# Optimization experiments

Measured on AMD Instinct MI355X. Metric: run time of the kernel, lower is better.

## Reference

```python
import jax, jax.numpy as jnp
import numpy as np

COORD_DIM = 2
ENTITY_DIM = 1024
FIELD_DIM = 512
INPUT_DIM = 512
NUM_ENTITIES = 512
FIELD_RESOLUTION = 10000  # grid_size = 100


def _gelu(x):
    return jax.nn.gelu(x, approximate=False)  # torch nn.GELU default (erf)


def setup_inputs() -> dict:
    key = jax.random.key(0)
    ks = jax.random.split(key, 9)
    std = 0.02  # matches _init_parameters
    B, S = 8, 4096
    x = jax.random.normal(ks[0], (B, S, INPUT_DIM), dtype=jnp.float32)
    # DensityField: density_projection = Linear(D,F) GELU Linear(F,F) GELU; coordinate_generator = Linear(F,2)
    W1 = jax.random.normal(ks[1], (INPUT_DIM, FIELD_DIM), jnp.float32) * std
    b1 = jnp.zeros((FIELD_DIM,), jnp.float32)
    W2 = jax.random.normal(ks[2], (FIELD_DIM, FIELD_DIM), jnp.float32) * std
    b2 = jnp.zeros((FIELD_DIM,), jnp.float32)
    Wc = jax.random.normal(ks[3], (FIELD_DIM, COORD_DIM), jnp.float32) * std
    bc = jnp.zeros((COORD_DIM,), jnp.float32)
    # entity_mapper: Linear(F+2, F) GELU Linear(F, E+2+1)
    We1 = jax.random.normal(ks[4], (FIELD_DIM + COORD_DIM, FIELD_DIM), jnp.float32) * std
    be1 = jnp.zeros((FIELD_DIM,), jnp.float32)
    We2 = jax.random.normal(ks[5], (FIELD_DIM, ENTITY_DIM + COORD_DIM + 1), jnp.float32) * std
    be2 = jnp.zeros((ENTITY_DIM + COORD_DIM + 1,), jnp.float32)
    # output_projection: Linear(E, 2E) GELU Linear(2E, D)
    Wo1 = jax.random.normal(ks[6], (ENTITY_DIM, 2 * ENTITY_DIM), jnp.float32) * std
    bo1 = jnp.zeros((2 * ENTITY_DIM,), jnp.float32)
    Wo2 = jax.random.normal(ks[7], (2 * ENTITY_DIM, INPUT_DIM), jnp.float32) * std
    bo2 = jnp.zeros((INPUT_DIM,), jnp.float32)
    return dict(x=x, W1=W1, b1=b1, W2=W2, b2=b2, Wc=Wc, bc=bc,
                We1=We1, be1=be1, We2=We2, be2=be2,
                Wo1=Wo1, bo1=bo1, Wo2=Wo2, bo2=bo2)


def _forward(x, W1, b1, W2, b2, Wc, bc, We1, be1, We2, be2, Wo1, bo1, Wo2, bo2):
    # --- DensityField ---
    df = _gelu(_gelu(x @ W1 + b1) @ W2 + b2)          # [B,S,F]
    coords = df @ Wc + bc                              # [B,S,2]
    # --- ContinuousEntityExtractor ---
    field_input = jnp.concatenate([coords, df], axis=-1)          # [B,S,2+F]
    ef = _gelu(field_input @ We1 + be1) @ We2 + be2                # [B,S,E+3]
    importance = jnp.linalg.norm(ef, axis=-1)                      # [B,S]
    _, top_idx = jax.lax.top_k(importance, NUM_ENTITIES)           # [B,Ne]
    sel = jnp.take_along_axis(ef, top_idx[..., None], axis=1)     # [B,Ne,E+3]
    positions = sel[..., :COORD_DIM]                               # [B,Ne,2]
    states = sel[..., COORD_DIM:COORD_DIM + ENTITY_DIM]            # [B,Ne,E]
    # --- ContinuousOutputGenerator ---
    proj = _gelu(states @ Wo1 + bo1) @ Wo2 + bo2                   # [B,Ne,D]
    grid_size = int(FIELD_RESOLUTION ** 0.5)
    g = jnp.linspace(-1.0, 1.0, grid_size)
    gx, gy = jnp.meshgrid(g, g, indexing='ij')
    grid = jnp.stack([gx.ravel(), gy.ravel()], axis=-1)            # [G2,2]
    # squared euclidean distances via expansion (torch: cdist then **2)
    g2 = jnp.sum(grid * grid, axis=-1)                             # [G2]
    p2 = jnp.sum(positions * positions, axis=-1)                   # [B,Ne]
    gp = jnp.einsum('gc,bnc->bgn', grid, positions)                # [B,G2,Ne]
    sq = g2[None, :, None] + p2[:, None, :] - 2.0 * gp             # [B,G2,Ne]
    attn = jnp.exp(-sq / 0.1)
    attn = attn / (attn.sum(axis=-1, keepdims=True) + 1e-8)
    out = jnp.einsum('bgn,bnd->bgd', attn, proj)                   # [B,G2,D]
    return out


def reference(x, W1, b1, W2, b2, Wc, bc, We1, be1, We2, be2, Wo1, bo1, Wo2, bo2):
    return _forward(x, W1, b1, W2, b2, Wc, bc, We1, be1, We2, be2, Wo1, bo1, Wo2, bo2)
```

## Files before the change

### kernel.cpp

```cpp
#include <hip/hip_runtime.h>
#include <hip/hip_bf16.h>
#include <math.h>


typedef __attribute__((ext_vector_type(8))) short bf16x8;
typedef __attribute__((ext_vector_type(4))) float f32x4;

__device__ __forceinline__ float gelu_exact(float x) {
    return 0.5f * x * (1.0f + erff(x * 0.7071067811865476f));
}

__device__ __forceinline__ void async_copy16(const void* g, void* l) {
    __builtin_amdgcn_global_load_lds(
        (const __attribute__((address_space(1))) unsigned int*)g,
        (__attribute__((address_space(3))) unsigned int*)l, 16, 0, 0);
}

__global__ __launch_bounds__(256) void split_kernel(
    const float* __restrict__ in,
    __hip_bfloat16* __restrict__ hi, __hip_bfloat16* __restrict__ lo)
{
    const int i4 = blockIdx.x * 256 + threadIdx.x;
    const float4 v = ((const float4*)in)[i4];
    __hip_bfloat16 h0 = __float2bfloat16(v.x);
    __hip_bfloat16 h1 = __float2bfloat16(v.y);
    __hip_bfloat16 h2 = __float2bfloat16(v.z);
    __hip_bfloat16 h3 = __float2bfloat16(v.w);
    __hip_bfloat16 l0 = __float2bfloat16(v.x - __bfloat162float(h0));
    __hip_bfloat16 l1 = __float2bfloat16(v.y - __bfloat162float(h1));
    __hip_bfloat16 l2 = __float2bfloat16(v.z - __bfloat162float(h2));
    __hip_bfloat16 l3 = __float2bfloat16(v.w - __bfloat162float(h3));
    union { __hip_bfloat16 h[4]; short4 s; } uh, ul;
    uh.h[0] = h0; uh.h[1] = h1; uh.h[2] = h2; uh.h[3] = h3;
    ul.h[0] = l0; ul.h[1] = l1; ul.h[2] = l2; ul.h[3] = l3;
    ((short4*)hi)[i4] = uh.s;
    ((short4*)lo)[i4] = ul.s;
}

__global__ __launch_bounds__(256) void transpose_split_kernel(
    const float* __restrict__ in,
    __hip_bfloat16* __restrict__ outH, __hip_bfloat16* __restrict__ outL,
    int K, int N)
{
    __shared__ float tile[32][33];
    const int k0 = blockIdx.y * 32, n0 = blockIdx.x * 32;
    const int t = threadIdx.x;
    const int lr = t >> 5, lc = t & 31;
    #pragma unroll
    for (int p = 0; p < 4; p++) {
        const int r = p * 8 + lr;
        const int n = n0 + lc;
        tile[r][lc] = (n < N) ? in[(size_t)(k0 + r) * N + n] : 0.f;
    }
    __syncthreads();
    #pragma unroll
    for (int p = 0; p < 4; p++) {
        const int r = p * 8 + lr;
        const float v = tile[lc][r];
        const __hip_bfloat16 h = __float2bfloat16(v);
        const __hip_bfloat16 l = __float2bfloat16(v - __bfloat162float(h));
        outH[(size_t)(n0 + r) * K + k0 + lc] = h;
        outL[(size_t)(n0 + r) * K + k0 + lc] = l;
    }
}

__global__ __launch_bounds__(256) void init_kernel(
    float* __restrict__ IMP, float* __restrict__ CRD,
    const float* __restrict__ bc)
{
    const int t = blockIdx.x * 256 + threadIdx.x;
    IMP[t] = 0.f;
    ((float2*)CRD)[t] = make_float2(bc[0], bc[1]);
}

template<bool GELU, bool RANK2, bool SPLIT, bool BOUNDS, int FUSE>
__global__ __launch_bounds__(256, 4) void gemm3k(
    const __hip_bfloat16* __restrict__ Ahi, const __hip_bfloat16* __restrict__ Alo,
    const __hip_bfloat16* __restrict__ Bhi, const __hip_bfloat16* __restrict__ Blo,
    const float* __restrict__ bias,
    float* __restrict__ Cf, int ldc,
    __hip_bfloat16* __restrict__ Chi, __hip_bfloat16* __restrict__ Clo,
    int N,
    const float* __restrict__ A2, const float* __restrict__ W2r,
    float* __restrict__ FO, const float* __restrict__ Wc)
{
    constexpr int K = 512;
    constexpr int NPS = K / 32;
    constexpr int NSTEPS = 3 * NPS;
    __shared__ __align__(16) __hip_bfloat16 As[2][128][32];
    __shared__ __align__(16) __hip_bfloat16 Bs[2][128][32];
    const int t = threadIdx.x;
    const int wave = t >> 6, lane = t & 63;
    const int wave_m = wave >> 1, wave_n = wave & 1;
    const int fr = lane & 15, quad = lane >> 4;
    const int gx = gridDim.x;
    const int nwg = gx * gridDim.y;
    int lid = blockIdx.y * gx + blockIdx.x;
    if ((nwg & 7) == 0) {
        const int chunk = nwg >> 3;
        lid = (lid & 7) * chunk + (lid >> 3);
    }
    const int m0 = (lid / gx) * 128;
    const int n0 = (lid % gx) * 128;
    const int srow = lane >> 2;
    const int skc  = (lane & 3) * 8;

    f32x4 acc[4][4] = {};

    auto STAGE = [&](int buf, int step) {
        int seg = 0, ts = step;
        if (ts >= NPS) { ts -= NPS; seg = 1; }
        if (ts >= NPS) { ts -= NPS; seg = 2; }
        const int kk = ts << 5;
        const __hip_bfloat16* Ab = (seg == 2) ? Alo : Ahi;
        const __hip_bfloat16* Bb = (seg == 1) ? Blo : Bhi;
        #pragma unroll
        for (int s = 0; s < 2; s++) {
            const int r = wave * 32 + s * 16 + srow;
            async_copy16(Ab + (size_t)(m0 + r) * K + kk + skc,
                         &As[buf][wave * 32 + s * 16][0]);
            async_copy16(Bb + (size_t)(n0 + r) * K + kk + skc,
                         &Bs[buf][wave * 32 + s * 16][0]);
        }
    };

    STAGE(0, 0);
    __syncthreads();
    int cur = 0;
    for (int step = 0; step < NSTEPS; ++step) {
        if (step + 1 < NSTEPS) STAGE(cur ^ 1, step + 1);
        bf16x8 af[4], bfv[4];
        #pragma unroll
        for (int i = 0; i < 4; i++)
            af[i] = *(const bf16x8*)&As[cur][wave_m * 64 + i * 16 + fr][quad * 8];
        #pragma unroll
        for (int j = 0; j < 4; j++)
            bfv[j] = *(const bf16x8*)&Bs[cur][wave_n * 64 + j * 16 + fr][quad * 8];
        #pragma unroll
        for (int i = 0; i < 4; i++)
            #pragma unroll
            for (int j = 0; j < 4; j++)
                acc[i][j] = __builtin_amdgcn_mfma_f32_16x16x32_bf16(
                    af[i], bfv[j], acc[i][j], 0, 0, 0);
        __syncthreads();
        cur ^= 1;
    }

    #pragma unroll
    for (int i = 0; i < 4; i++) {
        const int gmb = m0 + wave_m * 64 + i * 16 + quad * 4;
        float a2x[4], a2y[4];
        if (RANK2) {
            #pragma unroll
            for (int r = 0; r < 4; r++) {
                a2x[r] = A2[(size_t)(gmb + r) * 2];
                a2y[r] = A2[(size_t)(gmb + r) * 2 + 1];
            }
        }
        float f0[4] = {0.f, 0.f, 0.f, 0.f};
        float f1[4] = {0.f, 0.f, 0.f, 0.f};
        #pragma unroll
        for (int j = 0; j < 4; j++) {
            const int gn = n0 + wave_n * 64 + j * 16 + fr;
            const bool nok = !BOUNDS || (gn < N);
            const float bv = nok ? bias[gn] : 0.f;
            float w2a = 0.f, w2b = 0.f;
            if (RANK2) { w2a = W2r[gn]; w2b = W2r[512 + gn]; }
            float wcx = 0.f, wcy = 0.f;
            if (FUSE == 1) {
                const float2 wc = ((const float2*)Wc)[gn];
                wcx = wc.x; wcy = wc.y;
            }
            #pragma unroll
            for (int r = 0; r < 4; r++) {
                const int gm = gmb + r;
                float v = acc[i][j][r] + bv;
                if (RANK2) v += a2x[r] * w2a + a2y[r] * w2b;
                if (GELU) v = gelu_exact(v);
                if (SPLIT) {
                    const __hip_bfloat16 h = __float2bfloat16(v);
                    const __hip_bfloat16 l =
                        __float2bfloat16(v - __bfloat162float(h));
                    Chi[(size_t)gm * 512 + gn] = h;
                    Clo[(size_t)gm * 512 + gn] = l;
                } else if (nok) {
                    Cf[(size_t)gm * ldc + gn] = v;
                }
                if (FUSE == 1) { f0[r] += v * wcx; f1[r] += v * wcy; }
                if (FUSE == 2 && nok) f0[r] += v * v;
            }
        }
        if (FUSE) {
            #pragma unroll
            for (int r = 0; r < 4; r++) {
                float a = f0[r], b = f1[r];
                #pragma unroll
                for (int off = 1; off < 16; off <<= 1) {
                    a += __shfl_xor(a, off);
                    if (FUSE == 1) b += __shfl_xor(b, off);
                }
                if (fr == 0) {
                    if (FUSE == 1) {
                        atomicAdd(&FO[(size_t)(gmb + r) * 2],     a);
                        atomicAdd(&FO[(size_t)(gmb + r) * 2 + 1], b);
                    } else {
                        atomicAdd(&FO[gmb + r], a);
                    }
                }
            }
        }
    }
}

__global__ __launch_bounds__(1024) void topk_kernel(
    const float* __restrict__ IMP, int* __restrict__ IDX)
{
    __shared__ float v[4096];
    __shared__ int   ix[4096];
    const int b = blockIdx.x, t = threadIdx.x;
    for (int i = t; i < 4096; i += 1024) {
        v[i] = sqrtf(IMP[b * 4096 + i]);
        ix[i] = i;
    }
    __syncthreads();
    for (int k = 2; k <= 4096; k <<= 1) {
        for (int j = k >> 1; j > 0; j >>= 1) {
            for (int q = 0; q < 4; q++) {
                const int i = t + (q << 10);
                const int l = i ^ j;
                if (l > i) {
                    const float vi = v[i], vl = v[l];
                    const int   ii = ix[i], il = ix[l];
                    const bool after = (vi < vl) || (vi == vl && ii > il);
                    const bool dirAsc = ((i & k) == 0);
                    if (dirAsc ? after : !after) {
                        v[i] = vl; v[l] = vi; ix[i] = il; ix[l] = ii;
                    }
                }
            }
            __syncthreads();
        }
    }
    if (t < 512) IDX[b * 512 + t] = ix[t];
}

__global__ __launch_bounds__(256) void gather_kernel(
    const float* __restrict__ EF, const int* __restrict__ IDX,
    float* __restrict__ POS, __hip_bfloat16* __restrict__ ST)
{
    const int bn  = blockIdx.x;
    const int b   = bn >> 9;
    const int row = IDX[bn];
    const float* src = EF + ((size_t)(b * 4096) + row) * 1027;
    const int t = threadIdx.x;
    if (t < 2) POS[(size_t)bn * 2 + t] = src[t];
    __hip_bfloat16* dst = ST + (size_t)bn * 1024;
    for (int k = t; k < 1024; k += 256) dst[k] = __float2bfloat16(src[2 + k]);
}

__global__ __launch_bounds__(256) void transpose_cvt_kernel(
    const float* __restrict__ in, __hip_bfloat16* __restrict__ out,
    int K, int N)
{
    __shared__ float tile[32][33];
    const int k0 = blockIdx.y * 32, n0 = blockIdx.x * 32;
    const int t = threadIdx.x;
    const int lr = t >> 5, lc = t & 31;
    #pragma unroll
    for (int p = 0; p < 4; p++) {
        const int r = p * 8 + lr;
        tile[r][lc] = in[(size_t)(k0 + r) * N + n0 + lc];
    }
    __syncthreads();
    #pragma unroll
    for (int p = 0; p < 4; p++) {
        const int r = p * 8 + lr;
        out[(size_t)(n0 + r) * K + k0 + lc] = __float2bfloat16(tile[lc][r]);
    }
}

__global__ __launch_bounds__(256) void transpose_proj_kernel(
    const __hip_bfloat16* __restrict__ in, __hip_bfloat16* __restrict__ out)
{
    __shared__ __hip_bfloat16 tile[32][33];
    const int b = blockIdx.z;
    const int n0 = blockIdx.y * 32, d0 = blockIdx.x * 32;
    const int t = threadIdx.x;
    const int lr = t >> 5, lc = t & 31;
    #pragma unroll
    for (int p = 0; p < 4; p++) {
        const int r = p * 8 + lr;
        tile[r][lc] = in[((size_t)b * 512 + n0 + r) * 512 + d0 + lc];
    }
    __syncthreads();
    #pragma unroll
    for (int p = 0; p < 4; p++) {
        const int r = p * 8 + lr;
        out[((size_t)b * 512 + d0 + r) * 512 + n0 + lc] = tile[lc][r];
    }
}

template<bool GELU>
__global__ __launch_bounds__(256, 4) void gemm_post(
    const __hip_bfloat16* __restrict__ A,
    const __hip_bfloat16* __restrict__ BT,
    const float* __restrict__ bias,
    __hip_bfloat16* __restrict__ C,
    int N, int K)
{
    __shared__ __align__(16) __hip_bfloat16 As[2][128][32];
    __shared__ __align__(16) __hip_bfloat16 Bs[2][128][32];
    const int t = threadIdx.x;
    const int wave = t >> 6, lane = t & 63;
    const int wave_m = wave >> 1, wave_n = wave & 1;
    const int fr = lane & 15, quad = lane >> 4;
    const int gx = gridDim.x;
    const int nwg = gx * gridDim.y;
    int lid = blockIdx.y * gx + blockIdx.x;
    if ((nwg & 7) == 0) {
        const int chunk = nwg >> 3;
        lid = (lid & 7) * chunk + (lid >> 3);
    }
    const int m0 = (lid / gx) * 128;
    const int n0 = (lid % gx) * 128;
    const int srow = lane >> 2;
    const int skc  = (lane & 3) * 8;
    const int nsteps = K >> 5;

    f32x4 acc[4][4] = {};

    auto STAGE = [&](int buf, int step) {
        const int kk = step << 5;
        #pragma unroll
        for (int s = 0; s < 2; s++) {
            const int r = wave * 32 + s * 16 + srow;
            async_copy16(A  + (size_t)(m0 + r) * K + kk + skc,
                         &As[buf][wave * 32 + s * 16][0]);
            async_copy16(BT + (size_t)(n0 + r) * K + kk + skc,
                         &Bs[buf][wave * 32 + s * 16][0]);
        }
    };

    STAGE(0, 0);
    __syncthreads();
    int cur = 0;
    for (int step = 0; step < nsteps; ++step) {
        if (step + 1 < nsteps) STAGE(cur ^ 1, step + 1);
        bf16x8 af[4], bfv[4];
        #pragma unroll
        for (int i = 0; i < 4; i++)
            af[i] = *(const bf16x8*)&As[cur][wave_m * 64 + i * 16 + fr][quad * 8];
        #pragma unroll
        for (int j = 0; j < 4; j++)
            bfv[j] = *(const bf16x8*)&Bs[cur][wave_n * 64 + j * 16 + fr][quad * 8];
        #pragma unroll
        for (int i = 0; i < 4; i++)
            #pragma unroll
            for (int j = 0; j < 4; j++)
                acc[i][j] = __builtin_amdgcn_mfma_f32_16x16x32_bf16(
                    af[i], bfv[j], acc[i][j], 0, 0, 0);
        __syncthreads();
        cur ^= 1;
    }
    #pragma unroll
    for (int i = 0; i < 4; i++) {
        const int gm = m0 + wave_m * 64 + i * 16 + quad * 4;
        #pragma unroll
        for (int j = 0; j < 4; j++) {
            const int gn = n0 + wave_n * 64 + j * 16 + fr;
            const float bv = bias[gn];
            #pragma unroll
            for (int r = 0; r < 4; r++) {
                float v = acc[i][j][r] + bv;
                if (GELU) v = gelu_exact(v);
                C[(size_t)(gm + r) * N + gn] = __float2bfloat16(v);
            }
        }
    }
}

__global__ __launch_bounds__(256) void attn_mfma_kernel(
    const float* __restrict__ POS,
    const __hip_bfloat16* __restrict__ PROJT,
    float* __restrict__ OUT)
{
    __shared__ __align__(16) __hip_bfloat16 Bs[256][32];
    __shared__ float2 pos_s[512];
    __shared__ float srow_s[4][16];
    const int t = threadIdx.x;
    const int wave = t >> 6, lane = t & 63;
    const int fr = lane & 15, quad = lane >> 4;
    const int b  = blockIdx.z;
    const int g0 = blockIdx.x * 64;
    const int d0 = blockIdx.y * 256;

    {
        const float2* p = (const float2*)(POS + (size_t)b * 512 * 2);
        pos_s[t]       = p[t];
        pos_s[256 + t] = p[256 + t];
    }
    const int g = g0 + wave * 16 + fr;
    const bool gv = g < 10000;
    const float step = 2.0f / 99.0f;
    const int gi = gv ? (g / 100) : 0;
    const int gj = gv ? (g - gi * 100) : 0;
    const float gx = -1.f + step * (float)gi;
    const float gy = -1.f + step * (float)gj;

    f32x4 acc[16] = {};
    float wsum = 0.f;
    __syncthreads();

    for (int n0 = 0; n0 < 512; n0 += 32) {
        #pragma unroll
        for (int s = 0; s < 4; s++) {
            const int seg = wave * 4 + s;
            const __hip_bfloat16* gB = PROJT
                + ((size_t)b * 512 + d0 + seg * 16 + (lane >> 2)) * 512
                + n0 + (lane & 3) * 8;
            async_copy16(gB, &Bs[seg * 16][0]);
        }
        bf16x8 wf;
        float wl = 0.f;
        #pragma unroll
        for (int j = 0; j < 8; j++) {
            const int n = n0 + quad * 8 + j;
            const float2 pn = pos_s[n];
            const float dx = gx - pn.x, dy = gy - pn.y;
            const float w = gv ? __expf(-10.0f * (dx * dx + dy * dy)) : 0.f;
            const __hip_bfloat16 wb = __float2bfloat16(w);
            union { __hip_bfloat16 h; short s; } u; u.h = wb;
            wf[j] = u.s;
            wl += __bfloat162float(wb);
        }
        wsum += wl;
        __syncthreads();
        #pragma unroll
        for (int j = 0; j < 16; j++) {
            const bf16x8 bv = *(const bf16x8*)&Bs[j * 16 + fr][quad * 8];
            acc[j] = __builtin_amdgcn_mfma_f32_16x16x32_bf16(wf, bv, acc[j], 0, 0, 0);
        }
        __syncthreads();
    }
    wsum += __shfl_xor(wsum, 16);
    wsum += __shfl_xor(wsum, 32);
    if (lane < 16) srow_s[wave][lane] = wsum;
    __syncthreads();
    const int rbase = quad * 4;
    float inv[4];
    #pragma unroll
    for (int r = 0; r < 4; r++)
        inv[r] = 1.0f / (srow_s[wave][rbase + r] + 1e-8f);
    #pragma unroll
    for (int j = 0; j < 16; j++) {
        const int col = d0 + j * 16 + fr;
        #pragma unroll
        for (int r = 0; r < 4; r++) {
            const int gr = g0 + wave * 16 + rbase + r;
            if (gr < 10000)
                OUT[((size_t)b * 10000 + gr) * 512 + col] = acc[j][r] * inv[r];
        }
    }
}

extern "C" void kernel_launch(void* const* d_in, const int* in_sizes, int n_in,
                              void* d_out, int out_size, void* d_ws, size_t ws_size,
                              hipStream_t stream)
{
    const float* x   = (const float*)d_in[0];
    const float* W1  = (const float*)d_in[1];
    const float* b1  = (const float*)d_in[2];
    const float* W2  = (const float*)d_in[3];
    const float* b2  = (const float*)d_in[4];
    const float* Wc  = (const float*)d_in[5];
    const float* bc  = (const float*)d_in[6];
    const float* We1 = (const float*)d_in[7];
    const float* be1 = (const float*)d_in[8];
    const float* We2 = (const float*)d_in[9];
    const float* be2 = (const float*)d_in[10];
    const float* Wo1 = (const float*)d_in[11];
    const float* bo1 = (const float*)d_in[12];
    const float* Wo2 = (const float*)d_in[13];
    const float* bo2 = (const float*)d_in[14];
    float* out = (float*)d_out;

    const size_t BS = 32768;
    const size_t ACT = BS * 512;
    __hip_bfloat16* P0h = (__hip_bfloat16*)d_ws;
    __hip_bfloat16* P0l = P0h + ACT;
    __hip_bfloat16* P1h = P0l + ACT;
    __hip_bfloat16* P1l = P1h + ACT;
    float* EF  = (float*)(P1l + ACT);
    float* CRD = EF + BS * 1027;
    float* IMP = CRD + BS * 2;
    int*   IDX = (int*)(IMP + BS);
    float* POS = (float*)(IDX + 4096);
    __hip_bfloat16* W1Th = (__hip_bfloat16*)(POS + 4096 * 2);
    __hip_bfloat16* W1Tl = W1Th + 512 * 512;
    __hip_bfloat16* W2Th = W1Tl + 512 * 512;
    __hip_bfloat16* W2Tl = W2Th + 512 * 512;
    __hip_bfloat16* We1Th = W2Tl + 512 * 512;
    __hip_bfloat16* We1Tl = We1Th + 512 * 512;
    __hip_bfloat16* We2Th = We1Tl + 512 * 512;
    __hip_bfloat16* We2Tl = We2Th + (size_t)1152 * 512;
    __hip_bfloat16* ST    = P0h;
    __hip_bfloat16* H4    = ST + (size_t)4096 * 1024;
    __hip_bfloat16* PROJ  = H4 + (size_t)4096 * 2048;
    __hip_bfloat16* PROJT = PROJ + (size_t)4096 * 512;
    __hip_bfloat16* Wo1T  = PROJT + (size_t)4096 * 512;
    __hip_bfloat16* Wo2T  = Wo1T + (size_t)2048 * 1024;

    dim3 blk(256);
    split_kernel<<<dim3(16384), blk, 0, stream>>>(x, P0h, P0l);
    transpose_split_kernel<<<dim3(16, 16), blk, 0, stream>>>(W1, W1Th, W1Tl, 512, 512);
    transpose_split_kernel<<<dim3(16, 16), blk, 0, stream>>>(W2, W2Th, W2Tl, 512, 512);
    transpose_split_kernel<<<dim3(16, 16), blk, 0, stream>>>(We1 + 2 * 512, We1Th, We1Tl, 512, 512);
    transpose_split_kernel<<<dim3(36, 16), blk, 0, stream>>>(We2, We2Th, We2Tl, 512, 1027);
    init_kernel<<<dim3(128), blk, 0, stream>>>(IMP, CRD, bc);
    gemm3k<true, false, true, false, 0><<<dim3(4, 256), blk, 0, stream>>>(
        P0h, P0l, W1Th, W1Tl, b1, nullptr, 0, P1h, P1l, 512,
        nullptr, nullptr, nullptr, nullptr);
    gemm3k<true, false, true, false, 1><<<dim3(4, 256), blk, 0, stream>>>(
        P1h, P1l, W2Th, W2Tl, b2, nullptr, 0, P0h, P0l, 512,
        nullptr, nullptr, CRD, Wc);
    gemm3k<true, true, true, false, 0><<<dim3(4, 256), blk, 0, stream>>>(
        P0h, P0l, We1Th, We1Tl, be1, nullptr, 0, P1h, P1l, 512,
        CRD, We1, nullptr, nullptr);
    gemm3k<false, false, false, true, 2><<<dim3(9, 256), blk, 0, stream>>>(
        P1h, P1l, We2Th, We2Tl, be2, EF, 1027, nullptr, nullptr, 1027,
        nullptr, nullptr, IMP, nullptr);
    topk_kernel<<<dim3(8), dim3(1024), 0, stream>>>(IMP, IDX);
    transpose_cvt_kernel<<<dim3(64, 32), blk, 0, stream>>>(Wo1, Wo1T, 1024, 2048);
    transpose_cvt_kernel<<<dim3(16, 64), blk, 0, stream>>>(Wo2, Wo2T, 2048, 512);
    gather_kernel<<<dim3(4096), blk, 0, stream>>>(EF, IDX, POS, ST);
    gemm_post<true><<<dim3(16, 32), blk, 0, stream>>>(
        ST, Wo1T, bo1, H4, 2048, 1024);
    gemm_post<false><<<dim3(4, 32), blk, 0, stream>>>(
        H4, Wo2T, bo2, PROJ, 512, 2048);
    transpose_proj_kernel<<<dim3(16, 16, 8), blk, 0, stream>>>(PROJ, PROJT);
    attn_mfma_kernel<<<dim3(157, 2, 8), blk, 0, stream>>>(POS, PROJT, out);
}
```

Baseline: 898.4 us.

## Restructure split-bf16 GEMMs, store entity features as bf16, double-buffer attention

The 3-pass split-bf16 GEMM now loads hi and lo tiles of A and B together and issues all three MFMA products per K step, instead of running 48 sequential segments. This removes redundant hi tile reloads and the per-step segment logic, at the cost of double the LDS footprint and a launch-bounds occupancy hint lowered from 4 to 2. The last entity GEMM writes the 1024 state columns as bf16 and the coordinates separately, which shrinks the EF buffer and lets the gather kernel do a plain copy. All GEMMs switch to a fragment-contiguous LDS layout and wrap the MFMA block in s_setprio. The attention kernel gains double-buffered PROJT staging, which removes one barrier per iteration.

```diff
diff --git a/kernel.cpp b/kernel.cpp
--- a/kernel.cpp
+++ b/kernel.cpp
@@ -73,22 +73,21 @@
     ((float2*)CRD)[t] = make_float2(bc[0], bc[1]);
 }
 
-template<bool GELU, bool RANK2, bool SPLIT, bool BOUNDS, int FUSE>
-__global__ __launch_bounds__(256, 4) void gemm3k(
+template<bool GELU, bool RANK2, bool EFMODE, bool FUSEC>
+__global__ __launch_bounds__(256, 2) void gemm3k(
     const __hip_bfloat16* __restrict__ Ahi, const __hip_bfloat16* __restrict__ Alo,
     const __hip_bfloat16* __restrict__ Bhi, const __hip_bfloat16* __restrict__ Blo,
     const float* __restrict__ bias,
-    float* __restrict__ Cf, int ldc,
     __hip_bfloat16* __restrict__ Chi, __hip_bfloat16* __restrict__ Clo,
-    int N,
+    __hip_bfloat16* __restrict__ EFB, float* __restrict__ EFC,
+    float* __restrict__ IMP,
     const float* __restrict__ A2, const float* __restrict__ W2r,
-    float* __restrict__ FO, const float* __restrict__ Wc)
-{
-    constexpr int K = 512;
-    constexpr int NPS = K / 32;
-    constexpr int NSTEPS = 3 * NPS;
-    __shared__ __align__(16) __hip_bfloat16 As[2][128][32];
-    __shared__ __align__(16) __hip_bfloat16 Bs[2][128][32];
+    float* __restrict__ CRD, const float* __restrict__ Wc)
+{
+    __shared__ __align__(16) __hip_bfloat16 AsH[2][4096];
+    __shared__ __align__(16) __hip_bfloat16 AsL[2][4096];
+    __shared__ __align__(16) __hip_bfloat16 BsH[2][4096];
+    __shared__ __align__(16) __hip_bfloat16 BsL[2][4096];
     const int t = threadIdx.x;
     const int wave = t >> 6, lane = t & 63;
     const int wave_m = wave >> 1, wave_n = wave & 1;
@@ -96,52 +95,69 @@
     const int gx = gridDim.x;
     const int nwg = gx * gridDim.y;
     int lid = blockIdx.y * gx + blockIdx.x;
-    if ((nwg & 7) == 0) {
+    {
         const int chunk = nwg >> 3;
         lid = (lid & 7) * chunk + (lid >> 3);
     }
     const int m0 = (lid / gx) * 128;
     const int n0 = (lid % gx) * 128;
-    const int srow = lane >> 2;
-    const int skc  = (lane & 3) * 8;
+    const int lrow   = lane & 15;
+    const int lchunk = (lane >> 4) * 8;
 
     f32x4 acc[4][4] = {};
 
     auto STAGE = [&](int buf, int step) {
-        int seg = 0, ts = step;
-        if (ts >= NPS) { ts -= NPS; seg = 1; }
-        if (ts >= NPS) { ts -= NPS; seg = 2; }
-        const int kk = ts << 5;
-        const __hip_bfloat16* Ab = (seg == 2) ? Alo : Ahi;
-        const __hip_bfloat16* Bb = (seg == 1) ? Blo : Bhi;
+        const int kk = step << 5;
         #pragma unroll
         for (int s = 0; s < 2; s++) {
-            const int r = wave * 32 + s * 16 + srow;
-            async_copy16(Ab + (size_t)(m0 + r) * K + kk + skc,
-                         &As[buf][wave * 32 + s * 16][0]);
-            async_copy16(Bb + (size_t)(n0 + r) * K + kk + skc,
-                         &Bs[buf][wave * 32 + s * 16][0]);
+            const int seg = wave * 2 + s;
+            const size_t ao = (size_t)(m0 + seg * 16 + lrow) * 512 + kk + lchunk;
+            const size_t bo = (size_t)(n0 + seg * 16 + lrow) * 512 + kk + lchunk;
+            async_copy16(Ahi + ao, &AsH[buf][seg * 512]);
+            async_copy16(Alo + ao, &AsL[buf][seg * 512]);
+            async_copy16(Bhi + bo, &BsH[buf][seg * 512]);
+            async_copy16(Blo + bo, &BsL[buf][seg * 512]);
         }
     };
 
     STAGE(0, 0);
     __syncthreads();
     int cur = 0;
-    for (int step = 0; step < NSTEPS; ++step) {
-        if (step + 1 < NSTEPS) STAGE(cur ^ 1, step + 1);
-        bf16x8 af[4], bfv[4];
-        #pragma unroll
-        for (int i = 0; i < 4; i++)
-            af[i] = *(const bf16x8*)&As[cur][wave_m * 64 + i * 16 + fr][quad * 8];
-        #pragma unroll
-        for (int j = 0; j < 4; j++)
-            bfv[j] = *(const bf16x8*)&Bs[cur][wave_n * 64 + j * 16 + fr][quad * 8];
+    const int abase = wave_m * 2048 + quad * 128 + fr * 8;
+    const int bbase = wave_n * 2048 + quad * 128 + fr * 8;
+    for (int step = 0; step < 16; ++step) {
+        if (step + 1 < 16) STAGE(cur ^ 1, step + 1);
+        bf16x8 ah[4], al[4], bh[4], bl[4];
+        #pragma unroll
+        for (int i = 0; i < 4; i++) {
+            ah[i] = *(const bf16x8*)&AsH[cur][abase + i * 512];
+            al[i] = *(const bf16x8*)&AsL[cur][abase + i * 512];
+        }
+        #pragma unroll
+        for (int j = 0; j < 4; j++) {
+            bh[j] = *(const bf16x8*)&BsH[cur][bbase + j * 512];
+            bl[j] = *(const bf16x8*)&BsL[cur][bbase + j * 512];
+        }
+        __builtin_amdgcn_s_setprio(1);
         #pragma unroll
         for (int i = 0; i < 4; i++)
             #pragma unroll
             for (int j = 0; j < 4; j++)
                 acc[i][j] = __builtin_amdgcn_mfma_f32_16x16x32_bf16(
-                    af[i], bfv[j], acc[i][j], 0, 0, 0);
+                    ah[i], bh[j], acc[i][j], 0, 0, 0);
+        #pragma unroll
+        for (int i = 0; i < 4; i++)
+            #pragma unroll
+            for (int j = 0; j < 4; j++)
+                acc[i][j] = __builtin_amdgcn_mfma_f32_16x16x32_bf16(
+                    ah[i], bl[j], acc[i][j], 0, 0, 0);
+        #pragma unroll
+        for (int i = 0; i < 4; i++)
+            #pragma unroll
+            for (int j = 0; j < 4; j++)
+                acc[i][j] = __builtin_amdgcn_mfma_f32_16x16x32_bf16(
+                    al[i], bh[j], acc[i][j], 0, 0, 0);
+        __builtin_amdgcn_s_setprio(0);
         __syncthreads();
         cur ^= 1;
     }
@@ -162,12 +178,12 @@
         #pragma unroll
         for (int j = 0; j < 4; j++) {
             const int gn = n0 + wave_n * 64 + j * 16 + fr;
-            const bool nok = !BOUNDS || (gn < N);
+            const bool nok = !EFMODE || (gn < 1027);
             const float bv = nok ? bias[gn] : 0.f;
             float w2a = 0.f, w2b = 0.f;
             if (RANK2) { w2a = W2r[gn]; w2b = W2r[512 + gn]; }
             float wcx = 0.f, wcy = 0.f;
-            if (FUSE == 1) {
+            if (FUSEC) {
                 const float2 wc = ((const float2*)Wc)[gn];
                 wcx = wc.x; wcy = wc.y;
             }
@@ -177,34 +193,36 @@
                 float v = acc[i][j][r] + bv;
                 if (RANK2) v += a2x[r] * w2a + a2y[r] * w2b;
                 if (GELU) v = gelu_exact(v);
-                if (SPLIT) {
+                if (EFMODE) {
+                    if (gn < 2) EFC[(size_t)gm * 2 + gn] = v;
+                    else if (gn < 1026)
+                        EFB[(size_t)gm * 1024 + gn - 2] = __float2bfloat16(v);
+                    if (nok) f0[r] += v * v;
+                } else {
                     const __hip_bfloat16 h = __float2bfloat16(v);
                     const __hip_bfloat16 l =
                         __float2bfloat16(v - __bfloat162float(h));
                     Chi[(size_t)gm * 512 + gn] = h;
                     Clo[(size_t)gm * 512 + gn] = l;
-                } else if (nok) {
-                    Cf[(size_t)gm * ldc + gn] = v;
+                    if (FUSEC) { f0[r] += v * wcx; f1[r] += v * wcy; }
                 }
-                if (FUSE == 1) { f0[r] += v * wcx; f1[r] += v * wcy; }
-                if (FUSE == 2 && nok) f0[r] += v * v;
             }
         }
-        if (FUSE) {
+        if (EFMODE || FUSEC) {
             #pragma unroll
             for (int r = 0; r < 4; r++) {
                 float a = f0[r], b = f1[r];
                 #pragma unroll
                 for (int off = 1; off < 16; off <<= 1) {
                     a += __shfl_xor(a, off);
-                    if (FUSE == 1) b += __shfl_xor(b, off);
+                    if (FUSEC) b += __shfl_xor(b, off);
                 }
                 if (fr == 0) {
-                    if (FUSE == 1) {
-                        atomicAdd(&FO[(size_t)(gmb + r) * 2],     a);
-                        atomicAdd(&FO[(size_t)(gmb + r) * 2 + 1], b);
+                    if (FUSEC) {
+                        atomicAdd(&CRD[(size_t)(gmb + r) * 2],     a);
+                        atomicAdd(&CRD[(size_t)(gmb + r) * 2 + 1], b);
                     } else {
-                        atomicAdd(&FO[gmb + r], a);
+                        atomicAdd(&IMP[gmb + r], a);
                     }
                 }
             }
@@ -245,17 +263,20 @@
 }
 
 __global__ __launch_bounds__(256) void gather_kernel(
-    const float* __restrict__ EF, const int* __restrict__ IDX,
+    const __hip_bfloat16* __restrict__ EFB, const float* __restrict__ EFC,
+    const int* __restrict__ IDX,
     float* __restrict__ POS, __hip_bfloat16* __restrict__ ST)
 {
     const int bn  = blockIdx.x;
     const int b   = bn >> 9;
     const int row = IDX[bn];
-    const float* src = EF + ((size_t)(b * 4096) + row) * 1027;
-    const int t = threadIdx.x;
-    if (t < 2) POS[(size_t)bn * 2 + t] = src[t];
-    __hip_bfloat16* dst = ST + (size_t)bn * 1024;
-    for (int k = t; k < 1024; k += 256) dst[k] = __float2bfloat16(src[2 + k]);
+    const size_t src = (size_t)(b * 4096) + row;
+    const int t = threadIdx.x;
+    if (t < 2) POS[(size_t)bn * 2 + t] = EFC[src * 2 + t];
+    const unsigned int* s = (const unsigned int*)(EFB + src * 1024);
+    unsigned int* d = (unsigned int*)(ST + (size_t)bn * 1024);
+    d[t]       = s[t];
+    d[t + 256] = s[t + 256];
 }
 
 __global__ __launch_bounds__(256) void transpose_cvt_kernel(
@@ -308,8 +329,8 @@
     __hip_bfloat16* __restrict__ C,
     int N, int K)
 {
-    __shared__ __align__(16) __hip_bfloat16 As[2][128][32];
-    __shared__ __align__(16) __hip_bfloat16 Bs[2][128][32];
+    __shared__ __align__(16) __hip_bfloat16 As[2][4096];
+    __shared__ __align__(16) __hip_bfloat16 Bs[2][4096];
     const int t = threadIdx.x;
     const int wave = t >> 6, lane = t & 63;
     const int wave_m = wave >> 1, wave_n = wave & 1;
@@ -317,14 +338,14 @@
     const int gx = gridDim.x;
     const int nwg = gx * gridDim.y;
     int lid = blockIdx.y * gx + blockIdx.x;
-    if ((nwg & 7) == 0) {
+    {
         const int chunk = nwg >> 3;
         lid = (lid & 7) * chunk + (lid >> 3);
     }
     const int m0 = (lid / gx) * 128;
     const int n0 = (lid % gx) * 128;
-    const int srow = lane >> 2;
-    const int skc  = (lane & 3) * 8;
+    const int lrow   = lane & 15;
+    const int lchunk = (lane >> 4) * 8;
     const int nsteps = K >> 5;
 
     f32x4 acc[4][4] = {};
@@ -333,32 +354,36 @@
         const int kk = step << 5;
         #pragma unroll
         for (int s = 0; s < 2; s++) {
-            const int r = wave * 32 + s * 16 + srow;
-            async_copy16(A  + (size_t)(m0 + r) * K + kk + skc,
-                         &As[buf][wave * 32 + s * 16][0]);
-            async_copy16(BT + (size_t)(n0 + r) * K + kk + skc,
-                         &Bs[buf][wave * 32 + s * 16][0]);
+            const int seg = wave * 2 + s;
+            async_copy16(A  + (size_t)(m0 + seg * 16 + lrow) * K + kk + lchunk,
+                         &As[buf][seg * 512]);
+            async_copy16(BT + (size_t)(n0 + seg * 16 + lrow) * K + kk + lchunk,
+                         &Bs[buf][seg * 512]);
         }
     };
 
     STAGE(0, 0);
     __syncthreads();
     int cur = 0;
+    const int abase = wave_m * 2048 + quad * 128 + fr * 8;
+    const int bbase = wave_n * 2048 + quad * 128 + fr * 8;
     for (int step = 0; step < nsteps; ++step) {
         if (step + 1 < nsteps) STAGE(cur ^ 1, step + 1);
         bf16x8 af[4], bfv[4];
         #pragma unroll
         for (int i = 0; i < 4; i++)
-            af[i] = *(const bf16x8*)&As[cur][wave_m * 64 + i * 16 + fr][quad * 8];
+            af[i] = *(const bf16x8*)&As[cur][abase + i * 512];
         #pragma unroll
         for (int j = 0; j < 4; j++)
-            bfv[j] = *(const bf16x8*)&Bs[cur][wave_n * 64 + j * 16 + fr][quad * 8];
+            bfv[j] = *(const bf16x8*)&Bs[cur][bbase + j * 512];
+        __builtin_amdgcn_s_setprio(1);
         #pragma unroll
         for (int i = 0; i < 4; i++)
             #pragma unroll
             for (int j = 0; j < 4; j++)
                 acc[i][j] = __builtin_amdgcn_mfma_f32_16x16x32_bf16(
                     af[i], bfv[j], acc[i][j], 0, 0, 0);
+        __builtin_amdgcn_s_setprio(0);
         __syncthreads();
         cur ^= 1;
     }
@@ -384,7 +409,7 @@
     const __hip_bfloat16* __restrict__ PROJT,
     float* __restrict__ OUT)
 {
-    __shared__ __align__(16) __hip_bfloat16 Bs[256][32];
+    __shared__ __align__(16) __hip_bfloat16 Bs[2][8192];
     __shared__ float2 pos_s[512];
     __shared__ float srow_s[4][16];
     const int t = threadIdx.x;
@@ -393,6 +418,8 @@
     const int b  = blockIdx.z;
     const int g0 = blockIdx.x * 64;
     const int d0 = blockIdx.y * 256;
+    const int lrow   = lane & 15;
+    const int lchunk = (lane >> 4) * 8;
 
     {
         const float2* p = (const float2*)(POS + (size_t)b * 512 * 2);
@@ -407,19 +434,27 @@
     const float gx = -1.f + step * (float)gi;
     const float gy = -1.f + step * (float)gj;
 
-    f32x4 acc[16] = {};
-    float wsum = 0.f;
-    __syncthreads();
-
-    for (int n0 = 0; n0 < 512; n0 += 32) {
+    auto STAGE = [&](int buf, int n0s) {
         #pragma unroll
         for (int s = 0; s < 4; s++) {
             const int seg = wave * 4 + s;
             const __hip_bfloat16* gB = PROJT
-                + ((size_t)b * 512 + d0 + seg * 16 + (lane >> 2)) * 512
-                + n0 + (lane & 3) * 8;
-            async_copy16(gB, &Bs[seg * 16][0]);
-        }
+                + ((size_t)b * 512 + d0 + seg * 16 + lrow) * 512
+                + n0s + lchunk;
+            async_copy16(gB, &Bs[buf][seg * 512]);
+        }
+    };
+
+    f32x4 acc[16] = {};
+    float wsum = 0.f;
+    STAGE(0, 0);
+    __syncthreads();
+    int cur = 0;
+    const int bbase = quad * 128 + fr * 8;
+
+    for (int it = 0; it < 16; ++it) {
+        const int n0 = it * 32;
+        if (it + 1 < 16) STAGE(cur ^ 1, (it + 1) * 32);
         bf16x8 wf;
         float wl = 0.f;
         #pragma unroll
@@ -434,13 +469,15 @@
             wl += __bfloat162float(wb);
         }
         wsum += wl;
+        __builtin_amdgcn_s_setprio(1);
+        #pragma unroll
+        for (int j = 0; j < 16; j++) {
+            const bf16x8 bv = *(const bf16x8*)&Bs[cur][j * 512 + bbase];
+            acc[j] = __builtin_amdgcn_mfma_f32_16x16x32_bf16(wf, bv, acc[j], 0, 0, 0);
+        }
+        __builtin_amdgcn_s_setprio(0);
         __syncthreads();
-        #pragma unroll
-        for (int j = 0; j < 16; j++) {
-            const bf16x8 bv = *(const bf16x8*)&Bs[j * 16 + fr][quad * 8];
-            acc[j] = __builtin_amdgcn_mfma_f32_16x16x32_bf16(wf, bv, acc[j], 0, 0, 0);
-        }
-        __syncthreads();
+        cur ^= 1;
     }
     wsum += __shfl_xor(wsum, 16);
     wsum += __shfl_xor(wsum, 32);
@@ -490,8 +527,9 @@
     __hip_bfloat16* P0l = P0h + ACT;
     __hip_bfloat16* P1h = P0l + ACT;
     __hip_bfloat16* P1l = P1h + ACT;
-    float* EF  = (float*)(P1l + ACT);
-    float* CRD = EF + BS * 1027;
+    __hip_bfloat16* EFB = P1l + ACT;
+    float* EFC = (float*)(EFB + BS * 1024);
+    float* CRD = EFC + BS * 2;
     float* IMP = CRD + BS * 2;
     int*   IDX = (int*)(IMP + BS);
     float* POS = (float*)(IDX + 4096);
@@ -517,22 +555,22 @@
     transpose_split_kernel<<<dim3(16, 16), blk, 0, stream>>>(We1 + 2 * 512, We1Th, We1Tl, 512, 512);
     transpose_split_kernel<<<dim3(36, 16), blk, 0, stream>>>(We2, We2Th, We2Tl, 512, 1027);
     init_kernel<<<dim3(128), blk, 0, stream>>>(IMP, CRD, bc);
-    gemm3k<true, false, true, false, 0><<<dim3(4, 256), blk, 0, stream>>>(
-        P0h, P0l, W1Th, W1Tl, b1, nullptr, 0, P1h, P1l, 512,
-        nullptr, nullptr, nullptr, nullptr);
-    gemm3k<true, false, true, false, 1><<<dim3(4, 256), blk, 0, stream>>>(
-        P1h, P1l, W2Th, W2Tl, b2, nullptr, 0, P0h, P0l, 512,
-        nullptr, nullptr, CRD, Wc);
-    gemm3k<true, true, true, false, 0><<<dim3(4, 256), blk, 0, stream>>>(
-        P0h, P0l, We1Th, We1Tl, be1, nullptr, 0, P1h, P1l, 512,
-        CRD, We1, nullptr, nullptr);
-    gemm3k<false, false, false, true, 2><<<dim3(9, 256), blk, 0, stream>>>(
-        P1h, P1l, We2Th, We2Tl, be2, EF, 1027, nullptr, nullptr, 1027,
-        nullptr, nullptr, IMP, nullptr);
+    gemm3k<true, false, false, false><<<dim3(4, 256), blk, 0, stream>>>(
+        P0h, P0l, W1Th, W1Tl, b1, P1h, P1l,
+        nullptr, nullptr, nullptr, nullptr, nullptr, nullptr, nullptr);
+    gemm3k<true, false, false, true><<<dim3(4, 256), blk, 0, stream>>>(
+        P1h, P1l, W2Th, W2Tl, b2, P0h, P0l,
+        nullptr, nullptr, nullptr, nullptr, nullptr, CRD, Wc);
+    gemm3k<true, true, false, false><<<dim3(4, 256), blk, 0, stream>>>(
+        P0h, P0l, We1Th, We1Tl, be1, P1h, P1l,
+        nullptr, nullptr, nullptr, CRD, We1, nullptr, nullptr);
+    gemm3k<false, false, true, false><<<dim3(9, 256), blk, 0, stream>>>(
+        P1h, P1l, We2Th, We2Tl, be2, nullptr, nullptr,
+        EFB, EFC, IMP, nullptr, nullptr, nullptr, nullptr);
     topk_kernel<<<dim3(8), dim3(1024), 0, stream>>>(IMP, IDX);
     transpose_cvt_kernel<<<dim3(64, 32), blk, 0, stream>>>(Wo1, Wo1T, 1024, 2048);
     transpose_cvt_kernel<<<dim3(16, 64), blk, 0, stream>>>(Wo2, Wo2T, 2048, 512);
-    gather_kernel<<<dim3(4096), blk, 0, stream>>>(EF, IDX, POS, ST);
+    gather_kernel<<<dim3(4096), blk, 0, stream>>>(EFB, EFC, IDX, POS, ST);
     gemm_post<true><<<dim3(16, 32), blk, 0, stream>>>(
         ST, Wo1T, bo1, H4, 2048, 1024);
     gemm_post<false><<<dim3(4, 32), blk, 0, stream>>>(
```

After: 976.0 us. 1.09x slower.
